# Kernel optimization log

Measured on AMD Instinct MI355X. Metric: run time of the kernel, lower is better.

Reference implementation:

```python
import jax, jax.numpy as jnp
import numpy as np

B, C, S = 128, 32, 512          # batch, input_channel, seq_len (= d_model of the encoders)
EMB = 256                       # embed_size
NHEAD = 8                       # args.num_heads (also TransformerEncoderLayer nhead)
DFF = 2048                      # torch TransformerEncoderLayer default dim_feedforward
RLEN = S // 2 + 1               # 257 rfft bins
HK = int(RLEN * 0.5)            # 128, 'hight_freq_k' split point
LK = RLEN - HK                  # 129

def _ln(x, w, b, axes=-1):
    m = jnp.mean(x, axis=axes, keepdims=True)
    v = jnp.var(x, axis=axes, keepdims=True)
    return (x - m) / jnp.sqrt(v + 1e-5) * w + b

def _tel(x, in_w, in_b, out_w, out_b, ln1w, ln1b, w1, b1, w2, b2, ln2w, ln2b):
    # torch nn.TransformerEncoderLayer (batch_first, post-norm, relu, eval-mode dropout)
    b_, s_, d_ = x.shape
    dh = d_ // NHEAD
    qkv = x @ in_w.T + in_b
    q, k, v = jnp.split(qkv, 3, axis=-1)
    sp = lambda t: t.reshape(b_, s_, NHEAD, dh).transpose(0, 2, 1, 3)
    q, k, v = sp(q), sp(k), sp(v)
    sc = jnp.einsum('bhqd,bhkd->bhqk', q, k) / jnp.sqrt(jnp.asarray(dh, x.dtype))
    att = jax.nn.softmax(sc, axis=-1)
    o = jnp.einsum('bhqk,bhkd->bhqd', att, v).transpose(0, 2, 1, 3).reshape(b_, s_, d_)
    o = o @ out_w.T + out_b
    x = _ln(x + o, ln1w, ln1b)
    f = jax.nn.relu(x @ w1.T + b1) @ w2.T + b2
    return _ln(x + f, ln2w, ln2b)

def _crelu(z):
    return jax.lax.complex(jax.nn.relu(z.real), jax.nn.relu(z.imag))

def _csoftmax(z):
    return jax.lax.complex(jax.nn.softmax(z.real, axis=-1), jax.nn.softmax(z.imag, axis=-1))

def _cattn(q):
    # self-attention with complex Q=K=V (no conjugate, per torch matmul(Q, K^T))
    dk = q.shape[-1]
    sc = jnp.einsum('bqe,bke->bqk', q, q) / jnp.asarray(dk, jnp.float32) ** 0.5
    return jnp.einsum('bqk,bke->bqe', _csoftmax(sc), q)

def setup_inputs() -> dict:
    key = jax.random.key(0)
    ks = iter(jax.random.split(key, 64))
    n = lambda *sh: jax.random.normal(next(ks), sh, jnp.float32) * 0.02
    d = {'x': jax.random.normal(next(ks), (B, C, S), jnp.float32)}
    for p in ('t', 'r'):
        d[p + '_in_w'] = n(3 * S, S);  d[p + '_in_b'] = jnp.zeros((3 * S,), jnp.float32)
        d[p + '_out_w'] = n(S, S);     d[p + '_out_b'] = jnp.zeros((S,), jnp.float32)
        d[p + '_ln1_w'] = jnp.ones((S,), jnp.float32); d[p + '_ln1_b'] = jnp.zeros((S,), jnp.float32)
        d[p + '_lin1_w'] = n(DFF, S); d[p + '_lin1_b'] = jnp.zeros((DFF,), jnp.float32)
        d[p + '_lin2_w'] = n(S, DFF); d[p + '_lin2_b'] = jnp.zeros((S,), jnp.float32)
        d[p + '_ln2_w'] = jnp.ones((S,), jnp.float32); d[p + '_ln2_b'] = jnp.zeros((S,), jnp.float32)
    d['lc_w'] = n(S, S);  d['lc_b'] = jnp.zeros((S,), jnp.float32)
    d['up1_w'] = n(S, S); d['up1_b'] = jnp.zeros((S,), jnp.float32)
    d['up2_w'] = n(S, S); d['up2_b'] = jnp.zeros((S,), jnp.float32)
    d['n1_w'] = jnp.ones((C, S), jnp.float32); d['n1_b'] = jnp.zeros((C, S), jnp.float32)
    d['n2_w'] = jnp.ones((C, S), jnp.float32); d['n2_b'] = jnp.zeros((C, S), jnp.float32)
    d['l1_re'] = jax.random.normal(next(ks), (HK, EMB), jnp.float32)
    d['l1_im'] = jax.random.normal(next(ks), (HK, EMB), jnp.float32)
    d['h1_re'] = jax.random.normal(next(ks), (LK, EMB), jnp.float32)
    d['h1_im'] = jax.random.normal(next(ks), (LK, EMB), jnp.float32)
    d['lb1_re'] = jax.random.normal(next(ks), (EMB,), jnp.float32)
    d['lb1_im'] = jax.random.normal(next(ks), (EMB,), jnp.float32)
    d['hb1_re'] = jax.random.normal(next(ks), (EMB,), jnp.float32)
    d['hb1_im'] = jax.random.normal(next(ks), (EMB,), jnp.float32)
    return d

def reference(x, t_in_w, t_in_b, t_out_w, t_out_b, t_ln1_w, t_ln1_b, t_lin1_w, t_lin1_b, t_lin2_w, t_lin2_b, t_ln2_w, t_ln2_b, r_in_w, r_in_b, r_out_w, r_out_b, r_ln1_w, r_ln1_b, r_lin1_w, r_lin1_b, r_lin2_w, r_lin2_b, r_ln2_w, r_ln2_b, lc_w, lc_b, up1_w, up1_b, up2_w, up2_b, n1_w, n1_b, n2_w, n2_b, l1_re, l1_im, h1_re, h1_im, lb1_re, lb1_im, hb1_re, hb1_im):
    l1 = jax.lax.complex(l1_re, l1_im)
    h1 = jax.lax.complex(h1_re, h1_im)
    lb1 = jax.lax.complex(lb1_re, lb1_im)
    hb1 = jax.lax.complex(hb1_re, hb1_im)
    down_x = x  # downsample_scale=1 and padding_length=0 -> identity (i=0 path)
    # main branch
    df = jax.nn.relu(_tel(down_x, t_in_w, t_in_b, t_out_w, t_out_b, t_ln1_w, t_ln1_b,
                          t_lin1_w, t_lin1_b, t_lin2_w, t_lin2_b, t_ln2_w, t_ln2_b))
    df = _ln(df, n1_w, n1_b, axes=(-2, -1))
    # ttf_freqaug
    xf = jnp.fft.rfft(down_x, norm='ortho')                      # [B, C, 257] complex
    low = _crelu(jnp.einsum('bdk,ke->bde', xf[..., :HK], l1) + lb1)
    high = _crelu(jnp.einsum('bdk,ke->bde', xf[..., HK:], h1) + hb1)
    low = low + _cattn(low)
    high = high + _cattn(high)
    xcat = jnp.concatenate([low, high[..., low.shape[-1]:]], axis=-1)  # EMB bins (high slice is empty)
    fa = jnp.fft.irfft(xcat, n=S, norm='ortho')                  # zero-pads 256 -> 257 bins
    fa = fa @ lc_w.T + lc_b                                      # linear_change
    up = (fa @ up1_w.T + up1_b) @ up2_w.T + up2_b                # linear_up_sampling
    # recons branch
    rf = jax.nn.relu(_tel(fa, r_in_w, r_in_b, r_out_w, r_out_b, r_ln1_w, r_ln1_b,
                          r_lin1_w, r_lin1_b, r_lin2_w, r_lin2_b, r_ln2_w, r_ln2_b))
    rf = _ln(rf, n2_w, n2_b, axes=(-2, -1))
    res = df + rf
    return (res, down_x, fa, up)
```

## Files before the change

kernel.cpp:

```cpp
#include <hip/hip_runtime.h>
#include <math.h>


#define NROW 4096
#define NOUT 2097152

typedef __attribute__((ext_vector_type(8))) short short8;
typedef __attribute__((ext_vector_type(4))) float floatx4;

__device__ __forceinline__ unsigned short f2bf(float f) {
    union { float f; unsigned u; } v; v.f = f;
    return (unsigned short)((v.u + 0x7fffu + ((v.u >> 16) & 1u)) >> 16);
}
__device__ __forceinline__ float bf2f(unsigned short h) {
    union { unsigned u; float f; } v; v.u = ((unsigned)h) << 16;
    return v.f;
}

__device__ __forceinline__ void gload16(const unsigned short* g, unsigned short* l) {
    __builtin_amdgcn_global_load_lds((const __attribute__((address_space(1))) void*)g,
                                     (__attribute__((address_space(3))) void*)l, 16, 0, 0);
}

__device__ __forceinline__ void xcd_swizzle(int& bx, int& by, int& bz) {
    const int gx = gridDim.x, gy = gridDim.y;
    const int nwg = gx * gy * gridDim.z;
    int b = (bz * gy + by) * gx + bx;
    const int chunk = nwg >> 3;
    const int lb = (b & 7) * chunk + (b >> 3);
    bx = lb % gx;
    const int rem = lb / gx;
    by = rem % gy;
    bz = rem / gy;
}

__global__ __launch_bounds__(256) void tab_kernel(float* __restrict__ tabC, float* __restrict__ tabS)
{
    int n = blockIdx.x, k = threadIdx.x;
    int m = (n * k) & 511;
    float th = (float)m * 0.01227184630308513f;
    float s, c; sincosf(th, &s, &c);
    tabC[n * 256 + k] = c;
    tabS[n * 256 + k] = s;
}

__global__ __launch_bounds__(256) void wa_kernel(const float* __restrict__ l1_re, const float* __restrict__ l1_im,
                                                 const float* __restrict__ tabC, const float* __restrict__ tabS,
                                                 unsigned short* __restrict__ Wh, unsigned short* __restrict__ Wl)
{
    int n  = blockIdx.x;
    int ep = blockIdx.y * 256 + threadIdx.x;
    const float inv = 0.04419417382415922f;
    float acc = 0.f;
    if (ep < 256) {
        for (int k = 0; k < 128; ++k) {
            float c = tabC[n * 256 + k], s = tabS[n * 256 + k];
            acc += c * l1_re[k * 256 + ep] + s * l1_im[k * 256 + ep];
        }
    } else {
        int e = ep - 256;
        for (int k = 0; k < 128; ++k) {
            float c = tabC[n * 256 + k], s = tabS[n * 256 + k];
            acc += c * l1_im[k * 256 + e] - s * l1_re[k * 256 + e];
        }
    }
    float v = acc * inv;
    size_t idx = (size_t)ep * 512 + n;
    unsigned short h = f2bf(v);
    Wh[idx] = h;
    Wl[idx] = f2bf(v - bf2f(h));
}

__global__ __launch_bounds__(256) void wm_kernel(const float* __restrict__ lc_w,
                                                 const float* __restrict__ tabC, const float* __restrict__ tabS,
                                                 unsigned short* __restrict__ Wh, unsigned short* __restrict__ Wl)
{
    __shared__ float lw[512];
    int s  = blockIdx.x;
    int kk = blockIdx.y * 256 + threadIdx.x;
    for (int i = threadIdx.x; i < 512; i += 256) lw[i] = lc_w[s * 512 + i];
    __syncthreads();
    const float inv = 0.04419417382415922f;
    float acc = 0.f;
    if (kk < 256) {
        int k = kk;
        for (int n = 0; n < 512; ++n) acc += tabC[n * 256 + k] * lw[n];
        acc *= (k == 0) ? inv : 2.f * inv;
    } else {
        int k = kk - 256;
        if (k == 0) acc = 0.f;
        else {
            for (int n = 0; n < 512; ++n) acc += tabS[n * 256 + k] * lw[n];
            acc *= -2.f * inv;
        }
    }
    size_t idx = (size_t)s * 512 + kk;
    unsigned short h = f2bf(acc);
    Wh[idx] = h;
    Wl[idx] = f2bf(acc - bf2f(h));
}

__global__ __launch_bounds__(256) void lbpack_kernel(const float* __restrict__ re, const float* __restrict__ im,
                                                     float* __restrict__ out)
{
    int i = threadIdx.x + blockIdx.x * 256;
    if (i < 512) out[i] = (i < 256) ? re[i] : im[i - 256];
}

__global__ __launch_bounds__(256) void wcvt_kernel(
    const float* s0, const float* s1, const float* s2, const float* s3, const float* s4,
    const float* s5, const float* s6, const float* s7, const float* s8, const float* s9,
    unsigned short* __restrict__ o)
{
    int i = blockIdx.x * 256 + threadIdx.x;
    if (i >= 6815744) return;
    const float* s; int off;
    if (i < 3145728) {
        if (i < 1048576) { if (i < 786432) { s = s0; off = 0; } else { s = s1; off = 786432; } }
        else             { if (i < 2097152) { s = s2; off = 1048576; } else { s = s3; off = 2097152; } }
    } else {
        if (i < 5242880) {
            if (i < 3932160) { s = s4; off = 3145728; }
            else if (i < 4194304) { s = s5; off = 3932160; }
            else { s = s6; off = 4194304; }
        } else {
            if (i < 6291456) { s = s7; off = 5242880; }
            else if (i < 6553600) { s = s8; off = 6291456; }
            else { s = s9; off = 6553600; }
        }
    }
    o[i] = f2bf(s[i - off]);
}

__global__ __launch_bounds__(256) void cvt_lo_kernel(const float* __restrict__ a, const unsigned short* __restrict__ hi,
                                                     unsigned short* __restrict__ lo, int n)
{
    for (int i = blockIdx.x * 256 + threadIdx.x; i < n; i += gridDim.x * 256)
        lo[i] = f2bf(a[i] - bf2f(hi[i]));
}

__global__ __launch_bounds__(256) void xsplit_kernel(const float* __restrict__ a, unsigned short* __restrict__ hi,
                                                     unsigned short* __restrict__ lo, float* __restrict__ cp, int n)
{
    for (int i = blockIdx.x * 256 + threadIdx.x; i < n; i += gridDim.x * 256) {
        float v = a[i];
        unsigned short h = f2bf(v);
        hi[i] = h;
        lo[i] = f2bf(v - bf2f(h));
        cp[i] = v;
    }
}

template <int TM, int TN, int ACT, int WF, int WBF>
__global__ __launch_bounds__(256) void gemm_mfma(
    const unsigned short* __restrict__ A, const unsigned short* __restrict__ W,
    const float* __restrict__ bias, float* __restrict__ Cf,
    unsigned short* __restrict__ Cb, int N, int K)
{
    constexpr int MI = TM / 32, NJ = TN / 32;
    constexpr int ARW = TM / 4, BRW = TN / 4;
    __shared__ unsigned short As[2][TM * 32];
    __shared__ unsigned short Bs[2][TN * 32];
    const int tid = threadIdx.x;
    const int wave = tid >> 6, lane = tid & 63;
    int bx = blockIdx.x, by = blockIdx.y, bz = blockIdx.z;
    xcd_swizzle(bx, by, bz);
    const int m0 = by * TM, n0 = bx * TN;
    const int sr = lane >> 2, sc = (lane & 3) * 8;
    const unsigned short* aS = A + (size_t)(m0 + wave * ARW + sr) * K + sc;
    const unsigned short* wS = W + (size_t)(n0 + wave * BRW + sr) * K + sc;
    const int wm = (wave >> 1) * (TM / 2), wn = (wave & 1) * (TN / 2);
    const int fr = lane & 15, fko = (lane >> 4) * 8;

    floatx4 acc[MI][NJ];
#pragma unroll
    for (int i = 0; i < MI; ++i)
#pragma unroll
        for (int j = 0; j < NJ; ++j) acc[i][j] = (floatx4){0.f, 0.f, 0.f, 0.f};

    for (int k0 = 0; k0 < K; k0 += 64) {
#pragma unroll
        for (int h = 0; h < 2; ++h) {
#pragma unroll
            for (int c = 0; c < ARW / 16; ++c)
                gload16(aS + (size_t)(16 * c) * K + k0 + 32 * h, &As[h][(wave * ARW + 16 * c) * 32]);
#pragma unroll
            for (int c = 0; c < BRW / 16; ++c)
                gload16(wS + (size_t)(16 * c) * K + k0 + 32 * h, &Bs[h][(wave * BRW + 16 * c) * 32]);
        }
        __syncthreads();
#pragma unroll
        for (int h = 0; h < 2; ++h) {
            short8 af[MI], bfr[NJ];
#pragma unroll
            for (int i = 0; i < MI; ++i) af[i] = *(const short8*)&As[h][(wm + i * 16 + fr) * 32 + fko];
#pragma unroll
            for (int j = 0; j < NJ; ++j) bfr[j] = *(const short8*)&Bs[h][(wn + j * 16 + fr) * 32 + fko];
#pragma unroll
            for (int i = 0; i < MI; ++i)
#pragma unroll
                for (int j = 0; j < NJ; ++j)
                    acc[i][j] = __builtin_amdgcn_mfma_f32_16x16x32_bf16(af[i], bfr[j], acc[i][j], 0, 0, 0);
        }
        __syncthreads();
    }
    const int r0 = m0 + wm + (lane >> 4) * 4;
#pragma unroll
    for (int i = 0; i < MI; ++i) {
#pragma unroll
        for (int j = 0; j < NJ; ++j) {
            int n = n0 + wn + j * 16 + fr;
            float bv = bias[n];
#pragma unroll
            for (int r = 0; r < 4; ++r) {
                int m = r0 + i * 16 + r;
                size_t idx = (size_t)m * N + n;
                float v = acc[i][j][r] + bv;
                if (ACT) v = fmaxf(v, 0.f);
                if (WF) Cf[idx] = v;
                if (WBF) Cb[idx] = f2bf(v);
            }
        }
    }
}

template <int TM, int TN, int ACT, int WBF>
__global__ __launch_bounds__(256) void gemm_dual(
    const unsigned short* __restrict__ A0, const unsigned short* __restrict__ A1,
    const unsigned short* __restrict__ W0, const unsigned short* __restrict__ W1,
    const float* __restrict__ b0, const float* __restrict__ b1,
    float* __restrict__ C0, float* __restrict__ C1,
    unsigned short* __restrict__ D0, unsigned short* __restrict__ D1, int N, int K)
{
    constexpr int MI = TM / 32, NJ = TN / 32;
    constexpr int ARW = TM / 4, BRW = TN / 4;
    __shared__ unsigned short As[2][TM * 32];
    __shared__ unsigned short Bs[2][TN * 32];
    const int tid = threadIdx.x;
    const int wave = tid >> 6, lane = tid & 63;
    int bx = blockIdx.x, by = blockIdx.y, bz = blockIdx.z;
    xcd_swizzle(bx, by, bz);
    const int m0 = by * TM, n0 = bx * TN;
    const int z = bz;
    const unsigned short* A = z ? A1 : A0;
    const unsigned short* W = z ? W1 : W0;
    const float* bias = z ? b1 : b0;
    float* Cf = z ? C1 : C0;
    unsigned short* Cb = z ? D1 : D0;
    const int sr = lane >> 2, sc = (lane & 3) * 8;
    const unsigned short* aS = A + (size_t)(m0 + wave * ARW + sr) * K + sc;
    const unsigned short* wS = W + (size_t)(n0 + wave * BRW + sr) * K + sc;
    const int wm = (wave >> 1) * (TM / 2), wn = (wave & 1) * (TN / 2);
    const int fr = lane & 15, fko = (lane >> 4) * 8;

    floatx4 acc[MI][NJ];
#pragma unroll
    for (int i = 0; i < MI; ++i)
#pragma unroll
        for (int j = 0; j < NJ; ++j) acc[i][j] = (floatx4){0.f, 0.f, 0.f, 0.f};

    for (int k0 = 0; k0 < K; k0 += 64) {
#pragma unroll
        for (int h = 0; h < 2; ++h) {
#pragma unroll
            for (int c = 0; c < ARW / 16; ++c)
                gload16(aS + (size_t)(16 * c) * K + k0 + 32 * h, &As[h][(wave * ARW + 16 * c) * 32]);
#pragma unroll
            for (int c = 0; c < BRW / 16; ++c)
                gload16(wS + (size_t)(16 * c) * K + k0 + 32 * h, &Bs[h][(wave * BRW + 16 * c) * 32]);
        }
        __syncthreads();
#pragma unroll
        for (int h = 0; h < 2; ++h) {
            short8 af[MI], bfr[NJ];
#pragma unroll
            for (int i = 0; i < MI; ++i) af[i] = *(const short8*)&As[h][(wm + i * 16 + fr) * 32 + fko];
#pragma unroll
            for (int j = 0; j < NJ; ++j) bfr[j] = *(const short8*)&Bs[h][(wn + j * 16 + fr) * 32 + fko];
#pragma unroll
            for (int i = 0; i < MI; ++i)
#pragma unroll
                for (int j = 0; j < NJ; ++j)
                    acc[i][j] = __builtin_amdgcn_mfma_f32_16x16x32_bf16(af[i], bfr[j], acc[i][j], 0, 0, 0);
        }
        __syncthreads();
    }
    const int r0 = m0 + wm + (lane >> 4) * 4;
#pragma unroll
    for (int i = 0; i < MI; ++i) {
#pragma unroll
        for (int j = 0; j < NJ; ++j) {
            int n = n0 + wn + j * 16 + fr;
            float bv = bias[n];
#pragma unroll
            for (int r = 0; r < 4; ++r) {
                int m = r0 + i * 16 + r;
                size_t idx = (size_t)m * N + n;
                float v = acc[i][j][r] + bv;
                if (ACT) v = fmaxf(v, 0.f);
                if (WBF) Cb[idx] = f2bf(v);
                else     Cf[idx] = v;
            }
        }
    }
}

template <int TM, int TN, int ACT, int WCOPY, int WHILO>
__global__ __launch_bounds__(256) void gemm_mfma3(
    const unsigned short* __restrict__ Ah, const unsigned short* __restrict__ Al,
    const unsigned short* __restrict__ Wh, const unsigned short* __restrict__ Wl,
    const float* __restrict__ bias, float* __restrict__ Cf, float* __restrict__ Ccopy,
    unsigned short* __restrict__ Hh, unsigned short* __restrict__ Hl, int N, int K)
{
    constexpr int MI = TM / 32, NJ = TN / 32;
    constexpr int ARW = TM / 4, BRW = TN / 4;
    __shared__ unsigned short Ash[2][TM * 32];
    __shared__ unsigned short Asl[2][TM * 32];
    __shared__ unsigned short Bsh[2][TN * 32];
    __shared__ unsigned short Bsl[2][TN * 32];
    const int tid = threadIdx.x;
    const int wave = tid >> 6, lane = tid & 63;
    int bx = blockIdx.x, by = blockIdx.y, bz = blockIdx.z;
    xcd_swizzle(bx, by, bz);
    const int m0 = by * TM, n0 = bx * TN;
    const int sr = lane >> 2, sc = (lane & 3) * 8;
    const size_t aoff = (size_t)(m0 + wave * ARW + sr) * K + sc;
    const size_t woff = (size_t)(n0 + wave * BRW + sr) * K + sc;
    const int wm = (wave >> 1) * (TM / 2), wn = (wave & 1) * (TN / 2);
    const int fr = lane & 15, fko = (lane >> 4) * 8;

    floatx4 acc[MI][NJ];
#pragma unroll
    for (int i = 0; i < MI; ++i)
#pragma unroll
        for (int j = 0; j < NJ; ++j) acc[i][j] = (floatx4){0.f, 0.f, 0.f, 0.f};

    for (int k0 = 0; k0 < K; k0 += 64) {
#pragma unroll
        for (int h = 0; h < 2; ++h) {
#pragma unroll
            for (int c = 0; c < ARW / 16; ++c) {
                gload16(Ah + aoff + (size_t)(16 * c) * K + k0 + 32 * h, &Ash[h][(wave * ARW + 16 * c) * 32]);
                gload16(Al + aoff + (size_t)(16 * c) * K + k0 + 32 * h, &Asl[h][(wave * ARW + 16 * c) * 32]);
            }
#pragma unroll
            for (int c = 0; c < BRW / 16; ++c) {
                gload16(Wh + woff + (size_t)(16 * c) * K + k0 + 32 * h, &Bsh[h][(wave * BRW + 16 * c) * 32]);
                gload16(Wl + woff + (size_t)(16 * c) * K + k0 + 32 * h, &Bsl[h][(wave * BRW + 16 * c) * 32]);
            }
        }
        __syncthreads();
#pragma unroll
        for (int h = 0; h < 2; ++h) {
            short8 ah[MI], al[MI], bh[NJ], bl[NJ];
#pragma unroll
            for (int i = 0; i < MI; ++i) {
                ah[i] = *(const short8*)&Ash[h][(wm + i * 16 + fr) * 32 + fko];
                al[i] = *(const short8*)&Asl[h][(wm + i * 16 + fr) * 32 + fko];
            }
#pragma unroll
            for (int j = 0; j < NJ; ++j) {
                bh[j] = *(const short8*)&Bsh[h][(wn + j * 16 + fr) * 32 + fko];
                bl[j] = *(const short8*)&Bsl[h][(wn + j * 16 + fr) * 32 + fko];
            }
#pragma unroll
            for (int i = 0; i < MI; ++i)
#pragma unroll
                for (int j = 0; j < NJ; ++j) {
                    acc[i][j] = __builtin_amdgcn_mfma_f32_16x16x32_bf16(al[i], bh[j], acc[i][j], 0, 0, 0);
                    acc[i][j] = __builtin_amdgcn_mfma_f32_16x16x32_bf16(ah[i], bl[j], acc[i][j], 0, 0, 0);
                    acc[i][j] = __builtin_amdgcn_mfma_f32_16x16x32_bf16(ah[i], bh[j], acc[i][j], 0, 0, 0);
                }
        }
        __syncthreads();
    }
    const int r0 = m0 + wm + (lane >> 4) * 4;
#pragma unroll
    for (int i = 0; i < MI; ++i) {
#pragma unroll
        for (int j = 0; j < NJ; ++j) {
            int n = n0 + wn + j * 16 + fr;
            float bv = bias[n];
#pragma unroll
            for (int r = 0; r < 4; ++r) {
                int m = r0 + i * 16 + r;
                size_t idx = (size_t)m * N + n;
                float v = acc[i][j][r] + bv;
                if (ACT) v = fmaxf(v, 0.f);
                Cf[idx] = v;
                if (WCOPY) Ccopy[idx] = v;
                if (WHILO) {
                    unsigned short h = f2bf(v);
                    Hh[idx] = h;
                    Hl[idx] = f2bf(v - bf2f(h));
                }
            }
        }
    }
}

__global__ __launch_bounds__(256) void attn_dual_kernel(const float* __restrict__ qkvF,
                                                        const unsigned short* __restrict__ qkvB,
                                                        unsigned short* __restrict__ outR,
                                                        unsigned short* __restrict__ outT)
{
    const int isT = blockIdx.x >> 10;
    const int bid = blockIdx.x & 1023;
    const int b = bid >> 3;
    const int h = bid & 7;
    __shared__ float qs[32][65], ks[32][65], vs[32][65];
    __shared__ float ps[32][33];
    const int tid = threadIdx.x;
    if (isT) {
        for (int i = tid; i < 2048; i += 256) {
            int s = i >> 6, d = i & 63;
            size_t base = ((size_t)(b * 32 + s)) * 1536 + h * 64 + d;
            qs[s][d] = bf2f(qkvB[base]);
            ks[s][d] = bf2f(qkvB[base + 512]);
            vs[s][d] = bf2f(qkvB[base + 1024]);
        }
    } else {
        for (int i = tid; i < 2048; i += 256) {
            int s = i >> 6, d = i & 63;
            size_t base = ((size_t)(b * 32 + s)) * 1536 + h * 64 + d;
            qs[s][d] = qkvF[base];
            ks[s][d] = qkvF[base + 512];
            vs[s][d] = qkvF[base + 1024];
        }
    }
    __syncthreads();
    for (int i = tid; i < 1024; i += 256) {
        int si = i >> 5, sj = i & 31;
        float acc = 0.f;
#pragma unroll 8
        for (int d = 0; d < 64; ++d) acc += qs[si][d] * ks[sj][d];
        ps[si][sj] = acc * 0.125f;
    }
    __syncthreads();
    if (tid < 32) {
        float mx = -1e30f;
        for (int j = 0; j < 32; ++j) mx = fmaxf(mx, ps[tid][j]);
        float sum = 0.f;
        for (int j = 0; j < 32; ++j) { float e = __expf(ps[tid][j] - mx); ps[tid][j] = e; sum += e; }
        float inv = 1.f / sum;
        for (int j = 0; j < 32; ++j) ps[tid][j] *= inv;
    }
    __syncthreads();
    unsigned short* ob = isT ? outT : outR;
    for (int i = tid; i < 2048; i += 256) {
        int s = i >> 6, d = i & 63;
        float acc = 0.f;
#pragma unroll 8
        for (int k = 0; k < 32; ++k) acc += ps[s][k] * vs[k][d];
        ob[((size_t)(b * 32 + s)) * 512 + h * 64 + d] = f2bf(acc);
    }
}

__global__ __launch_bounds__(512) void cattn2_kernel(const float* __restrict__ LL,
                                                     unsigned short* __restrict__ outHi,
                                                     unsigned short* __restrict__ outLo)
{
    extern __shared__ float Xs[];
    __shared__ float Pr[16][33], Pi[16][33];
    const int b = blockIdx.x, half = blockIdx.y;
    const int tid = threadIdx.x;
    const float* base = LL + (size_t)b * 16384;
    for (int i = tid; i < 16384; i += 512) {
        int c = i >> 9, e = i & 511;
        Xs[e * 32 + ((c ^ e) & 31)] = base[i];
    }
    __syncthreads();
    {
        const int li = tid >> 5;
        const int ci = half * 16 + li;
        const int ck = tid & 31;
        float ar = 0.f, ai = 0.f;
#pragma unroll 4
        for (int er = 0; er < 256; ++er) {
            const int sw = er & 31;
            float yr = Xs[er * 32 + ((ck ^ sw) & 31)];
            float yi = Xs[(er + 256) * 32 + ((ck ^ sw) & 31)];
            float xr = Xs[er * 32 + ((ci ^ sw) & 31)];
            float xi = Xs[(er + 256) * 32 + ((ci ^ sw) & 31)];
            ar += xr * yr - xi * yi;
            ai += xr * yi + xi * yr;
        }
        Pr[li][ck] = ar * 0.0625f;
        Pi[li][ck] = ai * 0.0625f;
    }
    __syncthreads();
    if (tid < 32) {
        int r = tid & 15;
        float (*P)[33] = (tid < 16) ? Pr : Pi;
        float mx = -1e30f;
        for (int j = 0; j < 32; ++j) mx = fmaxf(mx, P[r][j]);
        float s = 0.f;
        for (int j = 0; j < 32; ++j) { float e = __expf(P[r][j] - mx); P[r][j] = e; s += e; }
        float inv = 1.f / s;
        for (int j = 0; j < 32; ++j) P[r][j] *= inv;
    }
    __syncthreads();
    const int er = tid & 255;
    const int th = tid >> 8;
    const int sw = er & 31;
    float accr[8], acci[8];
#pragma unroll
    for (int t = 0; t < 8; ++t) { accr[t] = 0.f; acci[t] = 0.f; }
    for (int k = 0; k < 32; ++k) {
        float yr = Xs[er * 32 + ((k ^ sw) & 31)];
        float yi = Xs[(er + 256) * 32 + ((k ^ sw) & 31)];
#pragma unroll
        for (int t = 0; t < 8; ++t) {
            float pr = Pr[th * 8 + t][k], pi = Pi[th * 8 + t][k];
            accr[t] += pr * yr - pi * yi;
            acci[t] += pr * yi + pi * yr;
        }
    }
#pragma unroll
    for (int t = 0; t < 8; ++t) {
        int c = half * 16 + th * 8 + t;
        float vr = Xs[er * 32 + ((c ^ sw) & 31)] + accr[t];
        float vi = Xs[(er + 256) * 32 + ((c ^ sw) & 31)] + acci[t];
        size_t ir = (size_t)b * 16384 + (size_t)c * 512 + er;
        unsigned short hr = f2bf(vr), hi2 = f2bf(vi);
        outHi[ir] = hr;        outLo[ir] = f2bf(vr - bf2f(hr));
        outHi[ir + 256] = hi2; outLo[ir + 256] = f2bf(vi - bf2f(hi2));
    }
}

__global__ __launch_bounds__(256) void add_ln_d1(
    const float* __restrict__ r0, const float* __restrict__ y0,
    const float* __restrict__ w0, const float* __restrict__ b0,
    unsigned short* __restrict__ h0, unsigned short* __restrict__ l0,
    const float* __restrict__ r1, const float* __restrict__ y1,
    const float* __restrict__ w1, const float* __restrict__ b1,
    unsigned short* __restrict__ h1, unsigned short* __restrict__ l1)
{
    const int row = blockIdx.x;
    const int br = row >> 12;
    const int rl = row & 4095;
    const float* resid = br ? r1 : r0;
    const float* y     = br ? y1 : y0;
    const float* w     = br ? w1 : w0;
    const float* bb    = br ? b1 : b0;
    unsigned short* oh = br ? h1 : h0;
    unsigned short* ol = br ? l1 : l0;
    const int tid = threadIdx.x;
    const size_t base = (size_t)rl * 512;
    float v0 = resid[base + tid] + y[base + tid];
    float v1 = resid[base + 256 + tid] + y[base + 256 + tid];
    float s = v0 + v1, q = v0 * v0 + v1 * v1;
    for (int off = 32; off; off >>= 1) { s += __shfl_down(s, off); q += __shfl_down(q, off); }
    __shared__ float sw[4], qw[4], ms, is;
    int wid = tid >> 6, lane = tid & 63;
    if (lane == 0) { sw[wid] = s; qw[wid] = q; }
    __syncthreads();
    if (tid == 0) {
        float S = sw[0] + sw[1] + sw[2] + sw[3];
        float Q = qw[0] + qw[1] + qw[2] + qw[3];
        float m = S * (1.f / 512.f);
        ms = m;
        is = rsqrtf(Q * (1.f / 512.f) - m * m + 1e-5f);
    }
    __syncthreads();
    float m = ms, inv = is;
    float o0 = (v0 - m) * inv * w[tid] + bb[tid];
    float o1 = (v1 - m) * inv * w[256 + tid] + bb[256 + tid];
    unsigned short e0 = f2bf(o0), e1 = f2bf(o1);
    oh[base + tid] = e0;       ol[base + tid] = f2bf(o0 - bf2f(e0));
    oh[base + 256 + tid] = e1; ol[base + 256 + tid] = f2bf(o1 - bf2f(e1));
}

__global__ __launch_bounds__(256) void add_ln_d2(
    const unsigned short* __restrict__ rh0, const unsigned short* __restrict__ rl0,
    const float* __restrict__ y0, const float* __restrict__ w0, const float* __restrict__ b0,
    float* __restrict__ o0p,
    const unsigned short* __restrict__ rh1, const unsigned short* __restrict__ rl1,
    const float* __restrict__ y1, const float* __restrict__ w1, const float* __restrict__ b1,
    float* __restrict__ o1p)
{
    const int row = blockIdx.x;
    const int br = row >> 12;
    const int rl = row & 4095;
    const unsigned short* rh = br ? rh1 : rh0;
    const unsigned short* rlo = br ? rl1 : rl0;
    const float* y  = br ? y1 : y0;
    const float* w  = br ? w1 : w0;
    const float* bb = br ? b1 : b0;
    float* op = br ? o1p : o0p;
    const int tid = threadIdx.x;
    const size_t base = (size_t)rl * 512;
    float v0 = bf2f(rh[base + tid]) + bf2f(rlo[base + tid]) + y[base + tid];
    float v1 = bf2f(rh[base + 256 + tid]) + bf2f(rlo[base + 256 + tid]) + y[base + 256 + tid];
    float s = v0 + v1, q = v0 * v0 + v1 * v1;
    for (int off = 32; off; off >>= 1) { s += __shfl_down(s, off); q += __shfl_down(q, off); }
    __shared__ float sw[4], qw[4], ms, is;
    int wid = tid >> 6, lane = tid & 63;
    if (lane == 0) { sw[wid] = s; qw[wid] = q; }
    __syncthreads();
    if (tid == 0) {
        float S = sw[0] + sw[1] + sw[2] + sw[3];
        float Q = qw[0] + qw[1] + qw[2] + qw[3];
        float m = S * (1.f / 512.f);
        ms = m;
        is = rsqrtf(Q * (1.f / 512.f) - m * m + 1e-5f);
    }
    __syncthreads();
    float m = ms, inv = is;
    op[base + tid]       = (v0 - m) * inv * w[tid] + bb[tid];
    op[base + 256 + tid] = (v1 - m) * inv * w[256 + tid] + bb[256 + tid];
}

template <int ADDF>
__global__ __launch_bounds__(256) void relu_bln_kernel(const float* __restrict__ xin,
                                                       const float* __restrict__ w, const float* __restrict__ b,
                                                       const float* __restrict__ addsrc,
                                                       float* __restrict__ out)
{
    const int bb = blockIdx.x;
    const int tid = threadIdx.x;
    const float* xp = xin + (size_t)bb * 16384;
    float s = 0.f, q = 0.f;
    for (int i = tid; i < 16384; i += 256) { float v = fmaxf(xp[i], 0.f); s += v; q += v * v; }
    for (int off = 32; off; off >>= 1) { s += __shfl_down(s, off); q += __shfl_down(q, off); }
    __shared__ float sw[4], qw[4], ms, is;
    int wid = tid >> 6, lane = tid & 63;
    if (lane == 0) { sw[wid] = s; qw[wid] = q; }
    __syncthreads();
    if (tid == 0) {
        float S = sw[0] + sw[1] + sw[2] + sw[3];
        float Q = qw[0] + qw[1] + qw[2] + qw[3];
        float m = S * (1.f / 16384.f);
        ms = m;
        is = rsqrtf(Q * (1.f / 16384.f) - m * m + 1e-5f);
    }
    __syncthreads();
    float m = ms, inv = is;
    const float* ap = ADDF ? (addsrc + (size_t)bb * 16384) : nullptr;
    float* op = out + (size_t)bb * 16384;
    for (int i = tid; i < 16384; i += 256) {
        float v = fmaxf(xp[i], 0.f);
        float o = (v - m) * inv * w[i] + b[i];
        if (ADDF) o += ap[i];
        op[i] = o;
    }
}

extern "C" void kernel_launch(void* const* d_in, const int* in_sizes, int n_in,
                              void* d_out, int out_size, void* d_ws, size_t ws_size,
                              hipStream_t stream)
{
    (void)in_sizes; (void)n_in; (void)out_size; (void)ws_size;
    const float* x        = (const float*)d_in[0];
    const float* t_in_w   = (const float*)d_in[1];
    const float* t_in_b   = (const float*)d_in[2];
    const float* t_out_w  = (const float*)d_in[3];
    const float* t_out_b  = (const float*)d_in[4];
    const float* t_ln1_w  = (const float*)d_in[5];
    const float* t_ln1_b  = (const float*)d_in[6];
    const float* t_lin1_w = (const float*)d_in[7];
    const float* t_lin1_b = (const float*)d_in[8];
    const float* t_lin2_w = (const float*)d_in[9];
    const float* t_lin2_b = (const float*)d_in[10];
    const float* t_ln2_w  = (const float*)d_in[11];
    const float* t_ln2_b  = (const float*)d_in[12];
    const float* r_in_w   = (const float*)d_in[13];
    const float* r_in_b   = (const float*)d_in[14];
    const float* r_out_w  = (const float*)d_in[15];
    const float* r_out_b  = (const float*)d_in[16];
    const float* r_ln1_w  = (const float*)d_in[17];
    const float* r_ln1_b  = (const float*)d_in[18];
    const float* r_lin1_w = (const float*)d_in[19];
    const float* r_lin1_b = (const float*)d_in[20];
    const float* r_lin2_w = (const float*)d_in[21];
    const float* r_lin2_b = (const float*)d_in[22];
    const float* r_ln2_w  = (const float*)d_in[23];
    const float* r_ln2_b  = (const float*)d_in[24];
    const float* lc_w     = (const float*)d_in[25];
    const float* lc_b     = (const float*)d_in[26];
    const float* up1_w    = (const float*)d_in[27];
    const float* up1_b    = (const float*)d_in[28];
    const float* up2_w    = (const float*)d_in[29];
    const float* up2_b    = (const float*)d_in[30];
    const float* n1_w     = (const float*)d_in[31];
    const float* n1_b     = (const float*)d_in[32];
    const float* n2_w     = (const float*)d_in[33];
    const float* n2_b     = (const float*)d_in[34];
    const float* l1_re    = (const float*)d_in[35];
    const float* l1_im    = (const float*)d_in[36];
    const float* lb1_re   = (const float*)d_in[39];
    const float* lb1_im   = (const float*)d_in[40];

    float* outp = (float*)d_out;

    float* WS   = (float*)d_ws;
    float* LL   = WS;
    float* FA   = WS;
    float* yR   = WS;
    float* QR   = WS + 2097152;
    float* tabC = QR;
    float* tabS = QR + 131072;
    unsigned short* WaHu = (unsigned short*)(QR + 786432);
    unsigned short* WaLu = (unsigned short*)(QR + 917504);
    unsigned short* WmHu = (unsigned short*)(QR + 1048576);
    unsigned short* WmLu = (unsigned short*)(QR + 1179648);
    float* qkvR = QR;
    unsigned short* x1rH = (unsigned short*)(WS + 2097152);
    unsigned short* x1rL = (unsigned short*)(WS + 3145728);
    unsigned short* x1tH = (unsigned short*)(WS + 4194304);
    unsigned short* x1tL = (unsigned short*)(WS + 5242880);
    float* yT   = WS + 6291456;
    unsigned short* qkvT = (unsigned short*)(WS + 8388608);
    unsigned short* f1R  = (unsigned short*)(WS + 8388608);
    float* x2R  = WS + 8388608;
    float* x2T  = WS + 10485760;
    unsigned short* xHi = (unsigned short*)(WS + 11534336);
    unsigned short* xLo = (unsigned short*)(WS + 12582912);
    unsigned short* aoR = (unsigned short*)(WS + 11534336);
    unsigned short* aoT = (unsigned short*)(WS + 12582912);
    unsigned short* f1T = (unsigned short*)(WS + 12582912);
    unsigned short* LLH = (unsigned short*)(WS + 13631488);
    unsigned short* LLL = (unsigned short*)(WS + 14680064);
    unsigned short* u1b = (unsigned short*)(WS + 13631488);
    float* oR   = WS + 13631488;
    float* oT   = WS + 15728640;
    unsigned short* faHi = (unsigned short*)(WS + 15728640);
    unsigned short* faLo = (unsigned short*)(WS + 16777216);
    unsigned short* rinLoU = (unsigned short*)(WS + 17825792);
    float* LB   = WS + 18219008;
    unsigned short* WB = (unsigned short*)(WS + 18366464);

    unsigned short* w_tin  = WB + 0;
    unsigned short* w_tout = WB + 786432;
    unsigned short* w_tl1  = WB + 1048576;
    unsigned short* w_tl2  = WB + 2097152;
    unsigned short* w_rin  = WB + 3145728;
    unsigned short* w_rout = WB + 3932160;
    unsigned short* w_rl1  = WB + 4194304;
    unsigned short* w_rl2  = WB + 5242880;
    unsigned short* w_up1  = WB + 6291456;
    unsigned short* w_up2  = WB + 6553600;

    dim3 blk(256);

    tab_kernel<<<dim3(512), blk, 0, stream>>>(tabC, tabS);
    wa_kernel<<<dim3(512, 2), blk, 0, stream>>>(l1_re, l1_im, tabC, tabS, WaHu, WaLu);
    wm_kernel<<<dim3(512, 2), blk, 0, stream>>>(lc_w, tabC, tabS, WmHu, WmLu);
    lbpack_kernel<<<dim3(2), blk, 0, stream>>>(lb1_re, lb1_im, LB);
    wcvt_kernel<<<dim3(26624), blk, 0, stream>>>(t_in_w, t_out_w, t_lin1_w, t_lin2_w,
                                                 r_in_w, r_out_w, r_lin1_w, r_lin2_w,
                                                 up1_w, up2_w, WB);
    xsplit_kernel<<<dim3(2048), blk, 0, stream>>>(x, xHi, xLo, outp + NOUT, NOUT);

    gemm_mfma3<64,64,1,0,0><<<dim3(8, 64), blk, 0, stream>>>(xHi, xLo, WaHu, WaLu, LB,
                                                             LL, nullptr, nullptr, nullptr, 512, 512);
    cattn2_kernel<<<dim3(128, 2), dim3(512), 65536, stream>>>(LL, LLH, LLL);
    gemm_mfma3<64,64,0,1,1><<<dim3(8, 64), blk, 0, stream>>>(LLH, LLL, WmHu, WmLu, lc_b,
                                                             FA, outp + 2 * NOUT, faHi, faLo, 512, 512);
    cvt_lo_kernel<<<dim3(768), blk, 0, stream>>>(r_in_w, w_rin, rinLoU, 786432);

    gemm_mfma<64,64,0,0,1><<<dim3(8, 64), blk, 0, stream>>>(faHi, w_up1, up1_b, nullptr, u1b, 512, 512);
    gemm_mfma<64,64,0,1,0><<<dim3(8, 64), blk, 0, stream>>>(u1b, w_up2, up2_b, outp + 3 * NOUT, nullptr, 512, 512);

    gemm_mfma3<64,128,0,0,0><<<dim3(12, 64), blk, 0, stream>>>(faHi, faLo, w_rin, rinLoU, r_in_b,
                                                               qkvR, nullptr, nullptr, nullptr, 1536, 512);
    gemm_mfma<64,128,0,0,1><<<dim3(12, 64), blk, 0, stream>>>(xHi, w_tin, t_in_b, nullptr, qkvT, 1536, 512);

    attn_dual_kernel<<<dim3(2048), blk, 0, stream>>>(qkvR, qkvT, aoR, aoT);
    gemm_dual<128,64,0,0><<<dim3(8, 32, 2), blk, 0, stream>>>(aoR, aoT, w_rout, w_tout,
                                                              r_out_b, t_out_b, oR, oT,
                                                              nullptr, nullptr, 512, 512);
    add_ln_d1<<<dim3(8192), blk, 0, stream>>>(FA, oR, r_ln1_w, r_ln1_b, x1rH, x1rL,
                                              x,  oT, t_ln1_w, t_ln1_b, x1tH, x1tL);
    gemm_dual<128,128,1,1><<<dim3(16, 32, 2), blk, 0, stream>>>(x1rH, x1tH, w_rl1, w_tl1,
                                                                r_lin1_b, t_lin1_b, nullptr, nullptr,
                                                                f1R, f1T, 2048, 512);
    gemm_dual<128,64,0,0><<<dim3(8, 32, 2), blk, 0, stream>>>(f1R, f1T, w_rl2, w_tl2,
                                                              r_lin2_b, t_lin2_b, yR, yT,
                                                              nullptr, nullptr, 512, 2048);
    add_ln_d2<<<dim3(8192), blk, 0, stream>>>(x1rH, x1rL, yR, r_ln2_w, r_ln2_b, x2R,
                                              x1tH, x1tL, yT, t_ln2_w, t_ln2_b, x2T);
    relu_bln_kernel<0><<<dim3(128), blk, 0, stream>>>(x2R, n2_w, n2_b, nullptr, x2R);
    relu_bln_kernel<1><<<dim3(128), blk, 0, stream>>>(x2T, n1_w, n1_b, x2R, outp);
}
```

Measured before the change: 523.9 us.

## Merge prep kernels, fuse dual QKV GEMM, shrink dual GEMM tiles, fuse final norms

Several small prep kernels are merged into two launches: a combined wa/wm weight builder and one prep kernel for weight conversion, r_in low part, x split and bias packing. The two QKV projections now share one launch, selected by the z index. The dual out-proj and FFN GEMMs move to smaller M tiles, giving a larger grid. The two relu+block-layernorm kernels become one 1024-thread kernel that keeps the recon result in shared memory. The aim is fewer launches and better occupancy, at the cost of more shared memory per block and a 64 KB LDS buffer in the fused norm.

After: 470.2 us. -10.3%, faster.

```diff
diff --git a/kernel.cpp b/kernel.cpp
--- a/kernel.cpp
+++ b/kernel.cpp
@@ -44,110 +44,100 @@
     tabS[n * 256 + k] = s;
 }
 
-__global__ __launch_bounds__(256) void wa_kernel(const float* __restrict__ l1_re, const float* __restrict__ l1_im,
-                                                 const float* __restrict__ tabC, const float* __restrict__ tabS,
-                                                 unsigned short* __restrict__ Wh, unsigned short* __restrict__ Wl)
-{
-    int n  = blockIdx.x;
-    int ep = blockIdx.y * 256 + threadIdx.x;
+__global__ __launch_bounds__(256) void wawm_kernel(const float* __restrict__ l1_re, const float* __restrict__ l1_im,
+                                                   const float* __restrict__ lc_w,
+                                                   const float* __restrict__ tabC, const float* __restrict__ tabS,
+                                                   unsigned short* __restrict__ WaH, unsigned short* __restrict__ WaL,
+                                                   unsigned short* __restrict__ WmH, unsigned short* __restrict__ WmL)
+{
+    __shared__ float lw[512];
     const float inv = 0.04419417382415922f;
-    float acc = 0.f;
-    if (ep < 256) {
-        for (int k = 0; k < 128; ++k) {
-            float c = tabC[n * 256 + k], s = tabS[n * 256 + k];
-            acc += c * l1_re[k * 256 + ep] + s * l1_im[k * 256 + ep];
-        }
+    if (blockIdx.z == 0) {
+        int n  = blockIdx.x;
+        int ep = blockIdx.y * 256 + threadIdx.x;
+        float acc = 0.f;
+        if (ep < 256) {
+            for (int k = 0; k < 128; ++k) {
+                float c = tabC[n * 256 + k], s = tabS[n * 256 + k];
+                acc += c * l1_re[k * 256 + ep] + s * l1_im[k * 256 + ep];
+            }
+        } else {
+            int e = ep - 256;
+            for (int k = 0; k < 128; ++k) {
+                float c = tabC[n * 256 + k], s = tabS[n * 256 + k];
+                acc += c * l1_im[k * 256 + e] - s * l1_re[k * 256 + e];
+            }
+        }
+        float v = acc * inv;
+        size_t idx = (size_t)ep * 512 + n;
+        unsigned short h = f2bf(v);
+        WaH[idx] = h;
+        WaL[idx] = f2bf(v - bf2f(h));
     } else {
-        int e = ep - 256;
-        for (int k = 0; k < 128; ++k) {
-            float c = tabC[n * 256 + k], s = tabS[n * 256 + k];
-            acc += c * l1_im[k * 256 + e] - s * l1_re[k * 256 + e];
-        }
-    }
-    float v = acc * inv;
-    size_t idx = (size_t)ep * 512 + n;
-    unsigned short h = f2bf(v);
-    Wh[idx] = h;
-    Wl[idx] = f2bf(v - bf2f(h));
-}
-
-__global__ __launch_bounds__(256) void wm_kernel(const float* __restrict__ lc_w,
-                                                 const float* __restrict__ tabC, const float* __restrict__ tabS,
-                                                 unsigned short* __restrict__ Wh, unsigned short* __restrict__ Wl)
-{
-    __shared__ float lw[512];
-    int s  = blockIdx.x;
-    int kk = blockIdx.y * 256 + threadIdx.x;
-    for (int i = threadIdx.x; i < 512; i += 256) lw[i] = lc_w[s * 512 + i];
-    __syncthreads();
-    const float inv = 0.04419417382415922f;
-    float acc = 0.f;
-    if (kk < 256) {
-        int k = kk;
-        for (int n = 0; n < 512; ++n) acc += tabC[n * 256 + k] * lw[n];
-        acc *= (k == 0) ? inv : 2.f * inv;
-    } else {
-        int k = kk - 256;
-        if (k == 0) acc = 0.f;
-        else {
-            for (int n = 0; n < 512; ++n) acc += tabS[n * 256 + k] * lw[n];
-            acc *= -2.f * inv;
-        }
-    }
-    size_t idx = (size_t)s * 512 + kk;
-    unsigned short h = f2bf(acc);
-    Wh[idx] = h;
-    Wl[idx] = f2bf(acc - bf2f(h));
-}
-
-__global__ __launch_bounds__(256) void lbpack_kernel(const float* __restrict__ re, const float* __restrict__ im,
-                                                     float* __restrict__ out)
-{
-    int i = threadIdx.x + blockIdx.x * 256;
-    if (i < 512) out[i] = (i < 256) ? re[i] : im[i - 256];
-}
-
-__global__ __launch_bounds__(256) void wcvt_kernel(
+        int s  = blockIdx.x;
+        int kk = blockIdx.y * 256 + threadIdx.x;
+        for (int i = threadIdx.x; i < 512; i += 256) lw[i] = lc_w[s * 512 + i];
+        __syncthreads();
+        float acc = 0.f;
+        if (kk < 256) {
+            int k = kk;
+            for (int n = 0; n < 512; ++n) acc += tabC[n * 256 + k] * lw[n];
+            acc *= (k == 0) ? inv : 2.f * inv;
+        } else {
+            int k = kk - 256;
+            if (k == 0) acc = 0.f;
+            else {
+                for (int n = 0; n < 512; ++n) acc += tabS[n * 256 + k] * lw[n];
+                acc *= -2.f * inv;
+            }
+        }
+        size_t idx = (size_t)s * 512 + kk;
+        unsigned short h = f2bf(acc);
+        WmH[idx] = h;
+        WmL[idx] = f2bf(acc - bf2f(h));
+    }
+}
+
+__global__ __launch_bounds__(256) void uber_prep_kernel(
     const float* s0, const float* s1, const float* s2, const float* s3, const float* s4,
     const float* s5, const float* s6, const float* s7, const float* s8, const float* s9,
-    unsigned short* __restrict__ o)
-{
-    int i = blockIdx.x * 256 + threadIdx.x;
-    if (i >= 6815744) return;
-    const float* s; int off;
-    if (i < 3145728) {
-        if (i < 1048576) { if (i < 786432) { s = s0; off = 0; } else { s = s1; off = 786432; } }
-        else             { if (i < 2097152) { s = s2; off = 1048576; } else { s = s3; off = 2097152; } }
+    unsigned short* __restrict__ o, unsigned short* __restrict__ rinLo,
+    const float* __restrict__ x, unsigned short* __restrict__ xhi,
+    unsigned short* __restrict__ xlo, float* __restrict__ xcp,
+    const float* __restrict__ lbre, const float* __restrict__ lbim, float* __restrict__ lbout)
+{
+    const int bid = blockIdx.x, tid = threadIdx.x;
+    if (bid < 26624) {
+        int i = bid * 256 + tid;
+        const float* s; int off;
+        if (i < 3145728) {
+            if (i < 1048576) { if (i < 786432) { s = s0; off = 0; } else { s = s1; off = 786432; } }
+            else             { if (i < 2097152) { s = s2; off = 1048576; } else { s = s3; off = 2097152; } }
+        } else {
+            if (i < 5242880) {
+                if (i < 3932160) { s = s4; off = 3145728; }
+                else if (i < 4194304) { s = s5; off = 3932160; }
+                else { s = s6; off = 4194304; }
+            } else {
+                if (i < 6291456) { s = s7; off = 5242880; }
+                else if (i < 6553600) { s = s8; off = 6291456; }
+                else { s = s9; off = 6553600; }
+            }
+        }
+        float v = s[i - off];
+        unsigned short h = f2bf(v);
+        o[i] = h;
+        if (i >= 3145728 && i < 3932160) rinLo[i - 3145728] = f2bf(v - bf2f(h));
+    } else if (bid < 34816) {
+        int i = (bid - 26624) * 256 + tid;
+        float v = x[i];
+        unsigned short h = f2bf(v);
+        xhi[i] = h;
+        xlo[i] = f2bf(v - bf2f(h));
+        xcp[i] = v;
     } else {
-        if (i < 5242880) {
-            if (i < 3932160) { s = s4; off = 3145728; }
-            else if (i < 4194304) { s = s5; off = 3932160; }
-            else { s = s6; off = 4194304; }
-        } else {
-            if (i < 6291456) { s = s7; off = 5242880; }
-            else if (i < 6553600) { s = s8; off = 6291456; }
-            else { s = s9; off = 6553600; }
-        }
-    }
-    o[i] = f2bf(s[i - off]);
-}
-
-__global__ __launch_bounds__(256) void cvt_lo_kernel(const float* __restrict__ a, const unsigned short* __restrict__ hi,
-                                                     unsigned short* __restrict__ lo, int n)
-{
-    for (int i = blockIdx.x * 256 + threadIdx.x; i < n; i += gridDim.x * 256)
-        lo[i] = f2bf(a[i] - bf2f(hi[i]));
-}
-
-__global__ __launch_bounds__(256) void xsplit_kernel(const float* __restrict__ a, unsigned short* __restrict__ hi,
-                                                     unsigned short* __restrict__ lo, float* __restrict__ cp, int n)
-{
-    for (int i = blockIdx.x * 256 + threadIdx.x; i < n; i += gridDim.x * 256) {
-        float v = a[i];
-        unsigned short h = f2bf(v);
-        hi[i] = h;
-        lo[i] = f2bf(v - bf2f(h));
-        cp[i] = v;
+        int i = (bid - 34816) * 256 + tid;
+        if (i < 512) lbout[i] = (i < 256) ? lbre[i] : lbim[i - 256];
     }
 }
 
@@ -399,6 +389,134 @@
     }
 }
 
+template <int TM, int TN>
+__global__ __launch_bounds__(256) void gemm_qkv_dual(
+    const unsigned short* __restrict__ Ah0, const unsigned short* __restrict__ Al0,
+    const unsigned short* __restrict__ Wh0, const unsigned short* __restrict__ Wl0,
+    const float* __restrict__ b0, float* __restrict__ C0,
+    const unsigned short* __restrict__ A1, const unsigned short* __restrict__ W1,
+    const float* __restrict__ b1, unsigned short* __restrict__ C1,
+    int N, int K)
+{
+    constexpr int MI = TM / 32, NJ = TN / 32;
+    constexpr int ARW = TM / 4, BRW = TN / 4;
+    __shared__ unsigned short Ash[2][TM * 32];
+    __shared__ unsigned short Asl[2][TM * 32];
+    __shared__ unsigned short Bsh[2][TN * 32];
+    __shared__ unsigned short Bsl[2][TN * 32];
+    const int tid = threadIdx.x;
+    const int wave = tid >> 6, lane = tid & 63;
+    int bx = blockIdx.x, by = blockIdx.y, bz = blockIdx.z;
+    xcd_swizzle(bx, by, bz);
+    const int m0 = by * TM, n0 = bx * TN;
+    const int sr = lane >> 2, sc = (lane & 3) * 8;
+    const size_t aoff = (size_t)(m0 + wave * ARW + sr) * K + sc;
+    const size_t woff = (size_t)(n0 + wave * BRW + sr) * K + sc;
+    const int wm = (wave >> 1) * (TM / 2), wn = (wave & 1) * (TN / 2);
+    const int fr = lane & 15, fko = (lane >> 4) * 8;
+
+    floatx4 acc[MI][NJ];
+#pragma unroll
+    for (int i = 0; i < MI; ++i)
+#pragma unroll
+        for (int j = 0; j < NJ; ++j) acc[i][j] = (floatx4){0.f, 0.f, 0.f, 0.f};
+
+    const int r0 = m0 + wm + (lane >> 4) * 4;
+
+    if (bz == 0) {
+        for (int k0 = 0; k0 < K; k0 += 64) {
+#pragma unroll
+            for (int h = 0; h < 2; ++h) {
+#pragma unroll
+                for (int c = 0; c < ARW / 16; ++c) {
+                    gload16(Ah0 + aoff + (size_t)(16 * c) * K + k0 + 32 * h, &Ash[h][(wave * ARW + 16 * c) * 32]);
+                    gload16(Al0 + aoff + (size_t)(16 * c) * K + k0 + 32 * h, &Asl[h][(wave * ARW + 16 * c) * 32]);
+                }
+#pragma unroll
+                for (int c = 0; c < BRW / 16; ++c) {
+                    gload16(Wh0 + woff + (size_t)(16 * c) * K + k0 + 32 * h, &Bsh[h][(wave * BRW + 16 * c) * 32]);
+                    gload16(Wl0 + woff + (size_t)(16 * c) * K + k0 + 32 * h, &Bsl[h][(wave * BRW + 16 * c) * 32]);
+                }
+            }
+            __syncthreads();
+#pragma unroll
+            for (int h = 0; h < 2; ++h) {
+                short8 ah[MI], al[MI], bh[NJ], bl[NJ];
+#pragma unroll
+                for (int i = 0; i < MI; ++i) {
+                    ah[i] = *(const short8*)&Ash[h][(wm + i * 16 + fr) * 32 + fko];
+                    al[i] = *(const short8*)&Asl[h][(wm + i * 16 + fr) * 32 + fko];
+                }
+#pragma unroll
+                for (int j = 0; j < NJ; ++j) {
+                    bh[j] = *(const short8*)&Bsh[h][(wn + j * 16 + fr) * 32 + fko];
+                    bl[j] = *(const short8*)&Bsl[h][(wn + j * 16 + fr) * 32 + fko];
+                }
+#pragma unroll
+                for (int i = 0; i < MI; ++i)
+#pragma unroll
+                    for (int j = 0; j < NJ; ++j) {
+                        acc[i][j] = __builtin_amdgcn_mfma_f32_16x16x32_bf16(al[i], bh[j], acc[i][j], 0, 0, 0);
+                        acc[i][j] = __builtin_amdgcn_mfma_f32_16x16x32_bf16(ah[i], bl[j], acc[i][j], 0, 0, 0);
+                        acc[i][j] = __builtin_amdgcn_mfma_f32_16x16x32_bf16(ah[i], bh[j], acc[i][j], 0, 0, 0);
+                    }
+            }
+            __syncthreads();
+        }
+#pragma unroll
+        for (int i = 0; i < MI; ++i)
+#pragma unroll
+            for (int j = 0; j < NJ; ++j) {
+                int n = n0 + wn + j * 16 + fr;
+                float bv = b0[n];
+#pragma unroll
+                for (int r = 0; r < 4; ++r) {
+                    int m = r0 + i * 16 + r;
+                    C0[(size_t)m * N + n] = acc[i][j][r] + bv;
+                }
+            }
+    } else {
+        for (int k0 = 0; k0 < K; k0 += 64) {
+#pragma unroll
+            for (int h = 0; h < 2; ++h) {
+#pragma unroll
+                for (int c = 0; c < ARW / 16; ++c)
+                    gload16(A1 + aoff + (size_t)(16 * c) * K + k0 + 32 * h, &Ash[h][(wave * ARW + 16 * c) * 32]);
+#pragma unroll
+                for (int c = 0; c < BRW / 16; ++c)
+                    gload16(W1 + woff + (size_t)(16 * c) * K + k0 + 32 * h, &Bsh[h][(wave * BRW + 16 * c) * 32]);
+            }
+            __syncthreads();
+#pragma unroll
+            for (int h = 0; h < 2; ++h) {
+                short8 af[MI], bfr[NJ];
+#pragma unroll
+                for (int i = 0; i < MI; ++i) af[i] = *(const short8*)&Ash[h][(wm + i * 16 + fr) * 32 + fko];
+#pragma unroll
+                for (int j = 0; j < NJ; ++j) bfr[j] = *(const short8*)&Bsh[h][(wn + j * 16 + fr) * 32 + fko];
+#pragma unroll
+                for (int i = 0; i < MI; ++i)
+#pragma unroll
+                    for (int j = 0; j < NJ; ++j)
+                        acc[i][j] = __builtin_amdgcn_mfma_f32_16x16x32_bf16(af[i], bfr[j], acc[i][j], 0, 0, 0);
+            }
+            __syncthreads();
+        }
+#pragma unroll
+        for (int i = 0; i < MI; ++i)
+#pragma unroll
+            for (int j = 0; j < NJ; ++j) {
+                int n = n0 + wn + j * 16 + fr;
+                float bv = b1[n];
+#pragma unroll
+                for (int r = 0; r < 4; ++r) {
+                    int m = r0 + i * 16 + r;
+                    C1[(size_t)m * N + n] = f2bf(acc[i][j][r] + bv);
+                }
+            }
+    }
+}
+
 __global__ __launch_bounds__(256) void attn_dual_kernel(const float* __restrict__ qkvF,
                                                         const unsigned short* __restrict__ qkvB,
                                                         unsigned short* __restrict__ outR,
@@ -611,38 +729,53 @@
     op[base + 256 + tid] = (v1 - m) * inv * w[256 + tid] + bb[256 + tid];
 }
 
-template <int ADDF>
-__global__ __launch_bounds__(256) void relu_bln_kernel(const float* __restrict__ xin,
-                                                       const float* __restrict__ w, const float* __restrict__ b,
-                                                       const float* __restrict__ addsrc,
-                                                       float* __restrict__ out)
-{
-    const int bb = blockIdx.x;
-    const int tid = threadIdx.x;
-    const float* xp = xin + (size_t)bb * 16384;
+__global__ __launch_bounds__(1024) void relu_bln_fused(
+    const float* __restrict__ xR, const float* __restrict__ w2, const float* __restrict__ b2,
+    const float* __restrict__ xT, const float* __restrict__ w1, const float* __restrict__ b1,
+    float* __restrict__ out)
+{
+    __shared__ float rfs[16384];
+    __shared__ float sw_[16], qw_[16], ms_, is_;
+    const int bb = blockIdx.x, tid = threadIdx.x;
+    const int wid = tid >> 6, lane = tid & 63;
+    const float* xr = xR + (size_t)bb * 16384;
     float s = 0.f, q = 0.f;
-    for (int i = tid; i < 16384; i += 256) { float v = fmaxf(xp[i], 0.f); s += v; q += v * v; }
+    for (int i = tid; i < 16384; i += 1024) { float v = fmaxf(xr[i], 0.f); s += v; q += v * v; }
     for (int off = 32; off; off >>= 1) { s += __shfl_down(s, off); q += __shfl_down(q, off); }
-    __shared__ float sw[4], qw[4], ms, is;
-    int wid = tid >> 6, lane = tid & 63;
-    if (lane == 0) { sw[wid] = s; qw[wid] = q; }
+    if (lane == 0) { sw_[wid] = s; qw_[wid] = q; }
     __syncthreads();
     if (tid == 0) {
-        float S = sw[0] + sw[1] + sw[2] + sw[3];
-        float Q = qw[0] + qw[1] + qw[2] + qw[3];
+        float S = 0.f, Q = 0.f;
+        for (int i = 0; i < 16; ++i) { S += sw_[i]; Q += qw_[i]; }
         float m = S * (1.f / 16384.f);
-        ms = m;
-        is = rsqrtf(Q * (1.f / 16384.f) - m * m + 1e-5f);
-    }
-    __syncthreads();
-    float m = ms, inv = is;
-    const float* ap = ADDF ? (addsrc + (size_t)bb * 16384) : nullptr;
+        ms_ = m;
+        is_ = rsqrtf(Q * (1.f / 16384.f) - m * m + 1e-5f);
+    }
+    __syncthreads();
+    float m = ms_, inv = is_;
+    for (int i = tid; i < 16384; i += 1024) {
+        float v = fmaxf(xr[i], 0.f);
+        rfs[i] = (v - m) * inv * w2[i] + b2[i];
+    }
+    const float* xt = xT + (size_t)bb * 16384;
+    s = 0.f; q = 0.f;
+    for (int i = tid; i < 16384; i += 1024) { float v = fmaxf(xt[i], 0.f); s += v; q += v * v; }
+    for (int off = 32; off; off >>= 1) { s += __shfl_down(s, off); q += __shfl_down(q, off); }
+    if (lane == 0) { sw_[wid] = s; qw_[wid] = q; }
+    __syncthreads();
+    if (tid == 0) {
+        float S = 0.f, Q = 0.f;
+        for (int i = 0; i < 16; ++i) { S += sw_[i]; Q += qw_[i]; }
+        float m2 = S * (1.f / 16384.f);
+        ms_ = m2;
+        is_ = rsqrtf(Q * (1.f / 16384.f) - m2 * m2 + 1e-5f);
+    }
+    __syncthreads();
+    m = ms_; inv = is_;
     float* op = out + (size_t)bb * 16384;
-    for (int i = tid; i < 16384; i += 256) {
-        float v = fmaxf(xp[i], 0.f);
-        float o = (v - m) * inv * w[i] + b[i];
-        if (ADDF) o += ap[i];
-        op[i] = o;
+    for (int i = tid; i < 16384; i += 1024) {
+        float v = fmaxf(xt[i], 0.f);
+        op[i] = (v - m) * inv * w1[i] + b1[i] + rfs[i];
     }
 }
 
@@ -744,42 +877,39 @@
     dim3 blk(256);
 
     tab_kernel<<<dim3(512), blk, 0, stream>>>(tabC, tabS);
-    wa_kernel<<<dim3(512, 2), blk, 0, stream>>>(l1_re, l1_im, tabC, tabS, WaHu, WaLu);
-    wm_kernel<<<dim3(512, 2), blk, 0, stream>>>(lc_w, tabC, tabS, WmHu, WmLu);
-    lbpack_kernel<<<dim3(2), blk, 0, stream>>>(lb1_re, lb1_im, LB);
-    wcvt_kernel<<<dim3(26624), blk, 0, stream>>>(t_in_w, t_out_w, t_lin1_w, t_lin2_w,
-                                                 r_in_w, r_out_w, r_lin1_w, r_lin2_w,
-                                                 up1_w, up2_w, WB);
-    xsplit_kernel<<<dim3(2048), blk, 0, stream>>>(x, xHi, xLo, outp + NOUT, NOUT);
+    wawm_kernel<<<dim3(512, 2, 2), blk, 0, stream>>>(l1_re, l1_im, lc_w, tabC, tabS,
+                                                     WaHu, WaLu, WmHu, WmLu);
+    uber_prep_kernel<<<dim3(34818), blk, 0, stream>>>(t_in_w, t_out_w, t_lin1_w, t_lin2_w,
+                                                      r_in_w, r_out_w, r_lin1_w, r_lin2_w,
+                                                      up1_w, up2_w, WB, rinLoU,
+                                                      x, xHi, xLo, outp + NOUT,
+                                                      lb1_re, lb1_im, LB);
 
     gemm_mfma3<64,64,1,0,0><<<dim3(8, 64), blk, 0, stream>>>(xHi, xLo, WaHu, WaLu, LB,
                                                              LL, nullptr, nullptr, nullptr, 512, 512);
     cattn2_kernel<<<dim3(128, 2), dim3(512), 65536, stream>>>(LL, LLH, LLL);
     gemm_mfma3<64,64,0,1,1><<<dim3(8, 64), blk, 0, stream>>>(LLH, LLL, WmHu, WmLu, lc_b,
                                                              FA, outp + 2 * NOUT, faHi, faLo, 512, 512);
-    cvt_lo_kernel<<<dim3(768), blk, 0, stream>>>(r_in_w, w_rin, rinLoU, 786432);
 
     gemm_mfma<64,64,0,0,1><<<dim3(8, 64), blk, 0, stream>>>(faHi, w_up1, up1_b, nullptr, u1b, 512, 512);
     gemm_mfma<64,64,0,1,0><<<dim3(8, 64), blk, 0, stream>>>(u1b, w_up2, up2_b, outp + 3 * NOUT, nullptr, 512, 512);
 
-    gemm_mfma3<64,128,0,0,0><<<dim3(12, 64), blk, 0, stream>>>(faHi, faLo, w_rin, rinLoU, r_in_b,
-                                                               qkvR, nullptr, nullptr, nullptr, 1536, 512);
-    gemm_mfma<64,128,0,0,1><<<dim3(12, 64), blk, 0, stream>>>(xHi, w_tin, t_in_b, nullptr, qkvT, 1536, 512);
+    gemm_qkv_dual<64,128><<<dim3(12, 64, 2), blk, 0, stream>>>(faHi, faLo, w_rin, rinLoU, r_in_b, qkvR,
+                                                               xHi, w_tin, t_in_b, qkvT, 1536, 512);
 
     attn_dual_kernel<<<dim3(2048), blk, 0, stream>>>(qkvR, qkvT, aoR, aoT);
-    gemm_dual<128,64,0,0><<<dim3(8, 32, 2), blk, 0, stream>>>(aoR, aoT, w_rout, w_tout,
-                                                              r_out_b, t_out_b, oR, oT,
-                                                              nullptr, nullptr, 512, 512);
+    gemm_dual<64,64,0,0><<<dim3(8, 64, 2), blk, 0, stream>>>(aoR, aoT, w_rout, w_tout,
+                                                             r_out_b, t_out_b, oR, oT,
+                                                             nullptr, nullptr, 512, 512);
     add_ln_d1<<<dim3(8192), blk, 0, stream>>>(FA, oR, r_ln1_w, r_ln1_b, x1rH, x1rL,
                                               x,  oT, t_ln1_w, t_ln1_b, x1tH, x1tL);
-    gemm_dual<128,128,1,1><<<dim3(16, 32, 2), blk, 0, stream>>>(x1rH, x1tH, w_rl1, w_tl1,
-                                                                r_lin1_b, t_lin1_b, nullptr, nullptr,
-                                                                f1R, f1T, 2048, 512);
-    gemm_dual<128,64,0,0><<<dim3(8, 32, 2), blk, 0, stream>>>(f1R, f1T, w_rl2, w_tl2,
-                                                              r_lin2_b, t_lin2_b, yR, yT,
-                                                              nullptr, nullptr, 512, 2048);
+    gemm_dual<64,128,1,1><<<dim3(16, 64, 2), blk, 0, stream>>>(x1rH, x1tH, w_rl1, w_tl1,
+                                                               r_lin1_b, t_lin1_b, nullptr, nullptr,
+                                                               f1R, f1T, 2048, 512);
+    gemm_dual<64,64,0,0><<<dim3(8, 64, 2), blk, 0, stream>>>(f1R, f1T, w_rl2, w_tl2,
+                                                             r_lin2_b, t_lin2_b, yR, yT,
+                                                             nullptr, nullptr, 512, 2048);
     add_ln_d2<<<dim3(8192), blk, 0, stream>>>(x1rH, x1rL, yR, r_ln2_w, r_ln2_b, x2R,
                                               x1tH, x1tL, yT, t_ln2_w, t_ln2_b, x2T);
-    relu_bln_kernel<0><<<dim3(128), blk, 0, stream>>>(x2R, n2_w, n2_b, nullptr, x2R);
-    relu_bln_kernel<1><<<dim3(128), blk, 0, stream>>>(x2T, n1_w, n1_b, x2R, outp);
-}
+    relu_bln_fused<<<dim3(128), dim3(1024), 0, stream>>>(x2R, n2_w, n2_b, x2T, n1_w, n1_b, outp);
+}
```
